# Kernel tuning notes

Hardware: AMD Instinct MI355X
Metric: run time of the kernel (lower is better)

The kernel has to match this reference:

```python
import jax, jax.numpy as jnp
import numpy as np

T, B, S, V = 50, 64, 400, 50000
D = 512; E = 512; H = 512; A = 512; POOL = 2


def setup_inputs() -> dict:
    key = jax.random.key(0)
    ks = jax.random.split(key, 20)
    def rn(k, shape, s=0.05):
        return jax.random.normal(k, shape, jnp.float32) * s
    return {
        "input_y": jax.random.randint(ks[0], (T, B), 0, V),
        "hidden": rn(ks[1], (1, B, H), 1.0),
        "context": rn(ks[2], (S, B, E), 1.0),
        "src_pad_mask": jnp.zeros((B, S), jnp.float32),
        "init_att": rn(ks[3], (B, E), 1.0),
        "coverage": jnp.zeros((B, S), jnp.float32),
        "global_ctx": rn(ks[4], (B, E), 1.0),
        "emb_W": rn(ks[5], (V, D)).at[0].set(0.0),  # padding_idx=0
        "W_ih": rn(ks[6], (3 * H, D + E)),
        "W_hh": rn(ks[7], (3 * H, H)),
        "b_ih": jnp.zeros((3 * H,), jnp.float32),
        "b_hh": jnp.zeros((3 * H,), jnp.float32),
        "W_pre": rn(ks[8], (E, A)),
        "b_pre": jnp.zeros((A,), jnp.float32),
        "W_q": rn(ks[9], (H + E, A)),
        "W_v": rn(ks[10], (A,)),
        "W_cov": rn(ks[11], (A,)),
        "W_pgen": rn(ks[12], (E + H + D,)),
        "b_pgen": jnp.zeros((), jnp.float32),
        "W_ro": rn(ks[13], (D + H + E + E, H)),
        "b_ro": jnp.zeros((H,), jnp.float32),
    }


def _gru_cell(x, h, W_ih, W_hh, b_ih, b_hh):
    # PyTorch GRUCell gate order: r, z, n
    gi = x @ W_ih.T + b_ih
    gh = h @ W_hh.T + b_hh
    i_r, i_z, i_n = jnp.split(gi, 3, axis=-1)
    h_r, h_z, h_n = jnp.split(gh, 3, axis=-1)
    r = jax.nn.sigmoid(i_r + h_r)
    z = jax.nn.sigmoid(i_z + h_z)
    n = jnp.tanh(i_n + r * h_n)
    return (1.0 - z) * n + z * h


def reference(input_y, hidden, context, src_pad_mask, init_att, coverage, global_ctx,
              emb_W, W_ih, W_hh, b_ih, b_hh, W_pre, b_pre, W_q, W_v, W_cov,
              W_pgen, b_pgen, W_ro, b_ro):
    emb = emb_W[input_y]                      # [T,B,D]
    ctx = jnp.transpose(context, (1, 0, 2))   # [B,S,E]
    precompute = ctx @ W_pre + b_pre          # [B,S,A] (computed once, as in module)
    pad = src_pad_mask > 0.5
    NEG = jnp.float32(-1e18)

    def step(carry, emb_t):
        h, cur_ctx, cov = carry
        x = jnp.concatenate([emb_t, cur_ctx], 1)          # input feed
        h0 = _gru_cell(x, h[0], W_ih, W_hh, b_ih, b_hh)   # layers=1
        h = h.at[0].set(h0)
        output = h0
        # concat attention with coverage
        q = jnp.concatenate([output, global_ctx], 1) @ W_q          # [B,A]
        tmp = jnp.tanh(precompute + q[:, None, :] + cov[..., None] * W_cov)
        energy = tmp @ W_v                                           # [B,S]
        energy = jnp.where(pad, NEG, energy)
        attn = jax.nn.softmax(energy, axis=1)
        cur_ctx = jnp.einsum('bs,bse->be', attn, ctx)
        # pointer-gen
        p_gen = jax.nn.sigmoid(
            jnp.concatenate([cur_ctx, output, emb_t], 1) @ W_pgen + b_pgen)[:, None]
        # readout + maxout (dropout is identity in eval)
        readout = jnp.concatenate([emb_t, output, cur_ctx, global_ctx], 1) @ W_ro + b_ro
        mo = readout.reshape(B, H // POOL, POOL).max(axis=-1)        # [B,H/POOL]
        cov_loss = jnp.sum(jnp.minimum(attn, cov), 1)                # cov_loss_wt=1.0
        next_cov = cov + attn
        return (h, cur_ctx, next_cov), (mo, p_gen, attn, cov_loss)

    (hidden_f, cur_ctx_f, cov_f), (g_out, g_pg, g_attn, cov_losses) = jax.lax.scan(
        step, (hidden, init_att, coverage), emb)
    return (g_out, hidden_f, g_attn[-1], cur_ctx_f, g_pg, g_attn, cov_losses, cov_f)
```

## Files before the change

### kernel.cpp

```cpp
#include <hip/hip_runtime.h>
#include <hip/hip_bf16.h>


#define T_STEPS 50
#define BB 64
#define SS 400

#define O_GOUT 0
#define O_HID 819200
#define O_ATTN_LAST 851968
#define O_CTXF 877568
#define O_PG 910336
#define O_GATTN 913536
#define O_COVL 2193536
#define O_COVF 2196736

typedef __attribute__((ext_vector_type(4))) float f4;
typedef __attribute__((ext_vector_type(8))) short s8v;
typedef __attribute__((ext_vector_type(4))) unsigned u4;

static __device__ __forceinline__ float bf2f(unsigned short u){
  unsigned v = ((unsigned)u) << 16; return __builtin_bit_cast(float, v);
}
static __device__ __forceinline__ unsigned short f2bf(float f){
  unsigned u = __builtin_bit_cast(unsigned, f);
  unsigned r = (u + 0x7FFFu + ((u >> 16) & 1u)) >> 16;
  return (unsigned short)r;
}
static __device__ __forceinline__ float sigmoidf_(float x){ return 1.f/(1.f+__expf(-x)); }
static __device__ __forceinline__ float tanhf_(float x){ float e=__expf(2.f*x); return 1.f - 2.f/(e+1.f); }
static __device__ __forceinline__ float ald32f(const float* p){
  unsigned u = __hip_atomic_load((const unsigned*)p, __ATOMIC_RELAXED, __HIP_MEMORY_SCOPE_AGENT);
  return __builtin_bit_cast(float, u);
}
static __device__ __forceinline__ void ast32f(float* p, float v){
  __hip_atomic_store((unsigned*)p, __builtin_bit_cast(unsigned, v),
                     __ATOMIC_RELAXED, __HIP_MEMORY_SCOPE_AGENT);
}

__global__ void conv_ctx(const float* __restrict__ ctx, unsigned short* __restrict__ out){
  int o = blockIdx.x*256 + threadIdx.x;
  if(o >= SS*BB*512) return;
  int e = o & 511; int b = (o>>9)&63; int s = o>>15;
  out[((b*SS+s)<<9) + e] = f2bf(ctx[o]);
}
__global__ void conv_emb(const int* __restrict__ y, const float* __restrict__ embW,
                         unsigned short* __restrict__ embU){
  int o = blockIdx.x*256+threadIdx.x; if(o>=T_STEPS*BB*512) return;
  int d = o & 511; int i = o>>9;
  embU[o] = f2bf(embW[(long)y[i]*512 + d]);
}
__global__ void conv_rest(const float* __restrict__ W_ih, const float* __restrict__ W_hh,
                          const float* __restrict__ W_pre, const float* __restrict__ W_ro,
                          const float* __restrict__ W_q,
                          const float* __restrict__ hidden, const float* __restrict__ init_att,
                          const float* __restrict__ gctx, const float* __restrict__ coverage,
                          unsigned short* __restrict__ wihbf, unsigned short* __restrict__ wpreT,
                          unsigned short* __restrict__ wroT, unsigned short* __restrict__ Wgru,
                          unsigned short* __restrict__ WqP,
                          float* __restrict__ hrow0, unsigned short* __restrict__ h0bf_init,
                          unsigned short* __restrict__ ctx0bf, float* __restrict__ gctxT,
                          float* __restrict__ cov, unsigned* __restrict__ flags){
  int o = blockIdx.x*256+threadIdx.x;
  if(o < 786432){
    int j = o>>9; int d = o&511;
    wihbf[o] = f2bf(W_ih[(long)j*1024 + d]);
  } else if(o < 1048576){
    int p = o - 786432;
    int a = p>>9; int e = p&511;
    wpreT[p] = f2bf(W_pre[(long)e*512 + a]);
  } else if(o < 2097152){
    int p = o - 1048576;
    int n = p>>11; int k = p&2047;
    wroT[p] = f2bf(W_ro[(long)k*512 + n]);
  } else if(o < 3670016){
    int p = o - 2097152;
    int rg = p >> 13; int rem = p & 8191;
    int ki = rem >> 9; int ln = (rem >> 3) & 63; int e = p & 7;
    int blk = rg/24; int r2 = rg%24; int w = r2/6; int r3 = r2%6; int g = r3>>1; int op = r3&1;
    int rl = ln & 15; int kk = ((ln>>4)<<3) + e;
    int d = blk*64 + w*16 + rl; int j = g*512 + d; int k = ki*32 + kk;
    float v = op ? W_hh[(long)j*512 + k] : W_ih[(long)j*1024 + 512 + k];
    Wgru[p] = f2bf(v);
  } else if(o < 3932160){
    int p = o - 3670016;
    int e = p&7; int ln=(p>>3)&63; int kf=(p>>9)&1; int nrg=(p>>10)&31; int blk=p>>15;
    int n = nrg*16 + (ln&15);
    int k = blk*64 + kf*32 + ((ln>>4)<<3) + e;
    WqP[p] = f2bf(W_q[(long)k*512 + n]);
  } else if(o < 4056128){
    int p = o - 3932160;
    if(p < 32768){ float v = hidden[p]; hrow0[p] = v; h0bf_init[p] = f2bf(v); }
    else if(p < 65536){ int q=p-32768; ctx0bf[q] = f2bf(init_att[q]); }
    else if(p < 98304){ int q=p-65536; int b=q>>9,e=q&511; gctxT[e*64+b]=gctx[q]; }
    else if(p < 123904){ int q=p-98304; cov[q]=coverage[q]; }
    else { int q=p-123904; if(q<64) flags[q]=0u; }
  }
}

template<int OUT_BF16>
__global__ __launch_bounds__(256) void mfma_gemm(
    const unsigned short* __restrict__ Abf, int lda,
    const unsigned short* __restrict__ Bbf, int ldb,
    void* __restrict__ Cp, int ldc, const float* __restrict__ bias, int K)
{
  __shared__ __align__(16) unsigned short Ash[128*40];
  __shared__ __align__(16) unsigned short Bsh[128*40];
  int m0 = blockIdx.x*128, n0 = blockIdx.y*128;
  int tid = threadIdx.x;
  int wid = tid>>6, lane = tid&63;
  int wm = wid>>1, wn = wid&1;
  int lr = lane&15, lg = lane>>4;
  f4 acc[4][4];
  #pragma unroll
  for(int i=0;i<4;i++)
    #pragma unroll
    for(int j=0;j<4;j++) acc[i][j]=(f4)0.f;

  for(int kt=0; kt<K; kt+=32){
    #pragma unroll
    for(int c=0;c<2;c++){
      int flat = tid*16 + c*8;
      int row = flat>>5, col = flat&31;
      const unsigned short* ga = Abf + (long)(m0+row)*lda + kt + col;
      *(uint4*)(&Ash[row*40+col]) = *(const uint4*)ga;
      const unsigned short* gb = Bbf + (long)(n0+row)*ldb + kt + col;
      *(uint4*)(&Bsh[row*40+col]) = *(const uint4*)gb;
    }
    __syncthreads();
    s8v av[4], bv[4];
    #pragma unroll
    for(int mi=0;mi<4;mi++) av[mi] = *(const s8v*)(&Ash[(wm*64+mi*16+lr)*40 + lg*8]);
    #pragma unroll
    for(int ni=0;ni<4;ni++) bv[ni] = *(const s8v*)(&Bsh[(wn*64+ni*16+lr)*40 + lg*8]);
    #pragma unroll
    for(int mi=0;mi<4;mi++)
      #pragma unroll
      for(int ni=0;ni<4;ni++)
        acc[mi][ni] = __builtin_amdgcn_mfma_f32_16x16x32_bf16(av[mi], bv[ni], acc[mi][ni], 0,0,0);
    __syncthreads();
  }
  #pragma unroll
  for(int mi=0;mi<4;mi++)
    #pragma unroll
    for(int ni=0;ni<4;ni++){
      int gc = n0 + wn*64 + ni*16 + lr;
      #pragma unroll
      for(int r=0;r<4;r++){
        int gr = m0 + wm*64 + mi*16 + lg*4 + r;
        float v = acc[mi][ni][r];
        if(bias) v += bias[gc];
        if(OUT_BF16) ((unsigned short*)Cp)[(long)gr*ldc + gc] = f2bf(v);
        else         ((float*)Cp)[(long)gr*ldc + gc] = v;
      }
    }
}

__global__ __launch_bounds__(256) void mfma_gemm_ro(
    const unsigned short* __restrict__ embU, const unsigned short* __restrict__ h0bf,
    const unsigned short* __restrict__ ctxA, const unsigned short* __restrict__ wroT,
    float* __restrict__ RO, const float* __restrict__ bias)
{
  __shared__ __align__(16) unsigned short Ash[128*40];
  __shared__ __align__(16) unsigned short Bsh[128*40];
  int m0 = blockIdx.x*128, n0 = blockIdx.y*128;
  int tid = threadIdx.x;
  int wid = tid>>6, lane = tid&63;
  int wm = wid>>1, wn = wid&1;
  int lr = lane&15, lg = lane>>4;
  f4 acc[4][4];
  #pragma unroll
  for(int i=0;i<4;i++)
    #pragma unroll
    for(int j=0;j<4;j++) acc[i][j]=(f4)0.f;

  for(int kt=0; kt<1536; kt+=32){
    const unsigned short* src = (kt<512) ? embU : (kt<1024) ? h0bf : ctxA;
    int klocal = kt & 511;
    #pragma unroll
    for(int c=0;c<2;c++){
      int flat = tid*16 + c*8;
      int row = flat>>5, col = flat&31;
      *(uint4*)(&Ash[row*40+col]) = *(const uint4*)(src + (long)(m0+row)*512 + klocal + col);
      *(uint4*)(&Bsh[row*40+col]) = *(const uint4*)(wroT + (long)(n0+row)*2048 + kt + col);
    }
    __syncthreads();
    s8v av[4], bv[4];
    #pragma unroll
    for(int mi=0;mi<4;mi++) av[mi] = *(const s8v*)(&Ash[(wm*64+mi*16+lr)*40 + lg*8]);
    #pragma unroll
    for(int ni=0;ni<4;ni++) bv[ni] = *(const s8v*)(&Bsh[(wn*64+ni*16+lr)*40 + lg*8]);
    #pragma unroll
    for(int mi=0;mi<4;mi++)
      #pragma unroll
      for(int ni=0;ni<4;ni++)
        acc[mi][ni] = __builtin_amdgcn_mfma_f32_16x16x32_bf16(av[mi], bv[ni], acc[mi][ni], 0,0,0);
    __syncthreads();
  }
  #pragma unroll
  for(int mi=0;mi<4;mi++)
    #pragma unroll
    for(int ni=0;ni<4;ni++){
      int gc = n0 + wn*64 + ni*16 + lr;
      #pragma unroll
      for(int r=0;r<4;r++){
        int gr = m0 + wm*64 + mi*16 + lg*4 + r;
        RO[(long)gr*512 + gc] = acc[mi][ni][r] + bias[gc];
      }
    }
}

__global__ __launch_bounds__(256) void small2(
  const float* __restrict__ AT, const float* __restrict__ W_q, const float* __restrict__ W_ro,
  float* __restrict__ q_g, float* __restrict__ ro_g)
{
  int blk = blockIdx.x;
  int half = blk>>7; int nblk = blk&127;
  int tid = threadIdx.x;
  int b = tid&63; int nq = tid>>6;
  int n = __builtin_amdgcn_readfirstlane(nblk*4 + nq);
  const float* W = half ? W_ro : W_q;
  int koff = half ? 1536 : 512;
  float acc = 0.f;
  const float* wp = W + (long)koff*512 + n;
  #pragma unroll 8
  for(int k=0;k<512;k++){
    acc = fmaf(AT[k*64+b], wp[(long)k*512], acc);
  }
  (half ? ro_g : q_g)[b*512+n] = acc;
}

__global__ __launch_bounds__(512) void k_step(
  const unsigned short* __restrict__ ctx0bf, float* __restrict__ ctxP,
  float* __restrict__ S_part, float* __restrict__ P_exp,
  const unsigned short* __restrict__ hprevbf,
  const float* __restrict__ hrow_in, float* __restrict__ hrow_out,
  const unsigned short* __restrict__ Wp, const unsigned short* __restrict__ WqP,
  const float* __restrict__ gi_emb, const float* __restrict__ b_hh,
  unsigned short* __restrict__ h0bf_all, float* __restrict__ qpart,
  float* __restrict__ cov, unsigned short* __restrict__ ctxA,
  const unsigned short* __restrict__ pre, const unsigned short* __restrict__ ctxbf,
  const float* __restrict__ q_g, const float* __restrict__ Wv,
  const float* __restrict__ Wcov, const float* __restrict__ padm,
  float* __restrict__ covl_part, unsigned* __restrict__ flags,
  float* __restrict__ outp, int t)
{
  __shared__ __align__(16) char smem[75008];
  const int blk = blockIdx.x;
  const int tid = threadIdx.x;
  const int w = tid>>6, lane = tid&63;
  const int lr = lane&15, lg = lane>>4;

  if(blk < 8){
    unsigned short* Ash = (unsigned short*)smem;
    unsigned short* HS  = (unsigned short*)(smem+65536);
    float* invS = (float*)(smem+74752);
    const int swz = (lr&7)<<4;
    const int dg = w&3, bh = w>>2;
    const int rgbase = blk*24 + dg*6;

    if(t>0 && tid<64){
      const float* Sp = S_part + ((t-1)&1)*256 + tid*4;
      invS[tid] = 1.f/(Sp[0]+Sp[1]+Sp[2]+Sp[3]);
    }
    __syncthreads();

    f4 acc2[6][2];
    #pragma unroll
    for(int u=0;u<6;u++)
      #pragma unroll
      for(int mm=0;mm<2;mm++) acc2[u][mm]=(f4)0.f;

    for(int kp=0; kp<2; kp++){
      for(int c = tid; c < 4096; c += 512){
        int op = c>>11; int row = (c>>5)&63; int kc = c&31;
        int e0 = kp*256 + kc*8;
        u4 v;
        if(op){
          v = *(const u4*)(hprevbf + row*512 + e0);
        } else if(t>0){
          const float* cp = ctxP + (long)row*2048 + e0;
          float sc = invS[row];
          f4 a0 = *(const f4*)(cp);
          f4 a1 = *(const f4*)(cp+512);
          f4 a2 = *(const f4*)(cp+1024);
          f4 a3 = *(const f4*)(cp+1536);
          f4 b0 = *(const f4*)(cp+4);
          f4 b1 = *(const f4*)(cp+516);
          f4 b2 = *(const f4*)(cp+1028);
          f4 b3 = *(const f4*)(cp+1540);
          f4 s0 = (a0+a1+a2+a3)*sc;
          f4 s1 = (b0+b1+b2+b3)*sc;
          v.x = (unsigned)f2bf(s0.x) | ((unsigned)f2bf(s0.y)<<16);
          v.y = (unsigned)f2bf(s0.z) | ((unsigned)f2bf(s0.w)<<16);
          v.z = (unsigned)f2bf(s1.x) | ((unsigned)f2bf(s1.y)<<16);
          v.w = (unsigned)f2bf(s1.z) | ((unsigned)f2bf(s1.w)<<16);
          if(blk == (row>>3))
            *(u4*)(ctxA + ((long)((t-1)*64+row))*512 + e0) = v;
        } else {
          v = *(const u4*)(ctx0bf + row*512 + e0);
        }
        int dst = op*32768 + row*512 + ((kc*16) ^ ((row&7)<<4));
        *(u4*)((char*)Ash + dst) = v;
      }
      __syncthreads();
      {
        #pragma unroll 2
        for(int ktl=0; ktl<256; ktl+=32){
          s8v av[2][2];
          #pragma unroll
          for(int op=0;op<2;op++)
            #pragma unroll
            for(int mm=0;mm<2;mm++){
              int mi = bh*2+mm;
              av[op][mm] = *(const s8v*)((const char*)Ash + op*32768 + (mi*16+lr)*512 + ((ktl*2 + lg*16) ^ swz));
            }
          int ki = kp*8 + (ktl>>5);
          const unsigned short* wb = Wp + (long)rgbase*8192 + ki*512 + lane*8;
          #pragma unroll
          for(int u=0;u<6;u++){
            s8v bv = *(const s8v*)(wb + (long)u*8192);
            #pragma unroll
            for(int mm=0;mm<2;mm++)
              acc2[u][mm] = __builtin_amdgcn_mfma_f32_16x16x32_bf16(av[u&1][mm], bv, acc2[u][mm], 0,0,0);
          }
        }
      }
      __syncthreads();
    }

    {
      int d = blk*64 + dg*16 + lr;
      float bhr = b_hh[d], bhz = b_hh[512+d], bhn = b_hh[1024+d];
      #pragma unroll
      for(int mm=0;mm<2;mm++){
        int mi = bh*2+mm;
        #pragma unroll
        for(int r=0;r<4;r++){
          int b = mi*16 + lg*4 + r;
          const float* ge = gi_emb + (long)(t*64+b)*1536;
          float g0 = __builtin_nontemporal_load(ge + d);
          float g1 = __builtin_nontemporal_load(ge + 512 + d);
          float g2 = __builtin_nontemporal_load(ge + 1024 + d);
          float rr = sigmoidf_(g0 + bhr + acc2[0][mm][r] + acc2[1][mm][r]);
          float zz = sigmoidf_(g1 + bhz + acc2[2][mm][r] + acc2[3][mm][r]);
          float nn = tanhf_(  g2       + acc2[4][mm][r] + rr*(acc2[5][mm][r] + bhn));
          float hp = hrow_in[b*512 + d];
          float hv = (1.f-zz)*nn + zz*hp;
          hrow_out[b*512+d] = hv;
          unsigned short hb = f2bf(hv);
          h0bf_all[(long)(t*64+b)*512 + d] = hb;
          HS[b*72 + dg*16 + lr] = hb;
          if(t==T_STEPS-1) outp[O_HID + b*512 + d] = hv;
        }
      }
    }
    __syncthreads();
    {
      #pragma unroll
      for(int i=0;i<8;i++){
        f4 accq[2];
        accq[0]=(f4)0.f; accq[1]=(f4)0.f;
        #pragma unroll
        for(int kf=0;kf<2;kf++){
          s8v bv = *(const s8v*)(WqP + ((((long)blk*32 + (dg*8+i))*2 + kf)*64 + lane)*8);
          #pragma unroll
          for(int mm=0;mm<2;mm++){
            int mi = bh*2+mm;
            s8v av = *(const s8v*)(HS + (mi*16+lr)*72 + kf*32 + lg*8);
            accq[mm] = __builtin_amdgcn_mfma_f32_16x16x32_bf16(av, bv, accq[mm], 0,0,0);
          }
        }
        int n = dg*128 + i*16 + lr;
        #pragma unroll
        for(int mm=0;mm<2;mm++)
          #pragma unroll
          for(int r=0;r<4;r++)
            ast32f(qpart + (long)blk*32768 + (long)((bh*2+mm)*16+lg*4+r)*512 + n, accq[mm][r]);
      }
    }
    asm volatile("s_waitcnt vmcnt(0)" ::: "memory");
    __syncthreads();
    if(tid==0)
      __hip_atomic_fetch_add(flags+t, 1u, __ATOMIC_RELEASE, __HIP_MEMORY_SCOPE_AGENT);
    return;
  }

  {
    int eb = blk-8; int b = eb>>2, cq = eb&3, c0 = cq*100;
    float* q_sh  = (float*)smem;
    float* wv_sh = (float*)(smem+2048);
    float* wc_sh = (float*)(smem+4096);
    float* covL  = (float*)(smem+6144);
    float* padL  = (float*)(smem+6560);
    float* red   = (float*)(smem+7392);
    float* red2  = (float*)(smem+9440);
    float* pb    = (float*)(smem+9472);

    wv_sh[tid]=Wv[tid]; wc_sh[tid]=Wcov[tid];
    if(tid<100) padL[tid]=padm[b*400+c0+tid];
    float clp = 0.f;
    if(t>0){
      const float* Sp = S_part + ((t-1)&1)*256 + b*4;
      float inv = 1.f/(Sp[0]+Sp[1]+Sp[2]+Sp[3]);
      if(tid<100){
        float p = P_exp[b*400+c0+tid]*inv;
        float co = cov[b*400+c0+tid];
        clp = fminf(p,co);
        float nc = co+p;
        cov[b*400+c0+tid]=nc;
        covL[tid]=nc;
        outp[O_GATTN + (long)(t-1)*25600 + b*400 + c0 + tid] = p;
      }
    } else {
      if(tid<100) covL[tid]=cov[b*400+c0+tid];
    }
    const unsigned short* prow = pre   + (((long)(b*400+c0))<<9) + lane*8;
    const unsigned short* crow = ctxbf + (((long)(b*400+c0))<<9) + lane*8;
    u4 pr[13], cr[13];
    #pragma unroll
    for(int j=0;j<13;j++){
      int i = w + j*8;
      long ro = (long)((i<100)? i : 0) << 9;
      pr[j] = *(const u4*)(prow + ro);
      cr[j] = *(const u4*)(crow + ro);
    }
    red[tid]=clp; __syncthreads();
    for(int o=256;o;o>>=1){ if(tid<o) red[tid]+=red[tid+o]; __syncthreads(); }
    if(t>0 && tid==0) covl_part[(long)(t-1)*256 + b*4+cq] = red[0];
    if(tid==0){
      unsigned it=0;
      while(__hip_atomic_load(flags+t, __ATOMIC_RELAXED, __HIP_MEMORY_SCOPE_AGENT) < 8u){
        __builtin_amdgcn_s_sleep(8);
        if(++it > 200000000u) break;
      }
    }
    __syncthreads();
    asm volatile("" ::: "memory");
    {
      float acc = q_g[b*512+tid];
      #pragma unroll
      for(int p=0;p<8;p++) acc += ald32f(qpart + ((long)p<<15) + b*512 + tid);
      q_sh[tid] = acc;
    }
    __syncthreads();
    float wsum = 0.f;
    float acc8[8];
    #pragma unroll
    for(int j=0;j<8;j++) acc8[j]=0.f;
    #pragma unroll
    for(int j=0;j<13;j++){
      int i = w + j*8;
      if(i<100){
        u4 cur = pr[j];
        const unsigned* uu = (const unsigned*)&cur;
        float cv = covL[i];
        float part = 0.f;
        #pragma unroll
        for(int q4=0;q4<4;q4++){
          int a = lane*8 + q4*2;
          part += wv_sh[a]  * tanhf_(bf2f((unsigned short)(uu[q4]&0xffffu)) + q_sh[a]   + cv*wc_sh[a]);
          part += wv_sh[a+1]* tanhf_(bf2f((unsigned short)(uu[q4]>>16))    + q_sh[a+1] + cv*wc_sh[a+1]);
        }
        #pragma unroll
        for(int off=32;off;off>>=1) part += __shfl_xor(part, off, 64);
        float e = (padL[i]>0.5f) ? -1e18f : part;
        float p = __expf(e);
        if(lane==0) P_exp[b*400+c0+i] = p;
        wsum += p;
        u4 cc = cr[j];
        const unsigned* cu = (const unsigned*)&cc;
        acc8[0] = fmaf(p, bf2f((unsigned short)(cu[0]&0xffffu)), acc8[0]);
        acc8[1] = fmaf(p, bf2f((unsigned short)(cu[0]>>16)),     acc8[1]);
        acc8[2] = fmaf(p, bf2f((unsigned short)(cu[1]&0xffffu)), acc8[2]);
        acc8[3] = fmaf(p, bf2f((unsigned short)(cu[1]>>16)),     acc8[3]);
        acc8[4] = fmaf(p, bf2f((unsigned short)(cu[2]&0xffffu)), acc8[4]);
        acc8[5] = fmaf(p, bf2f((unsigned short)(cu[2]>>16)),     acc8[5]);
        acc8[6] = fmaf(p, bf2f((unsigned short)(cu[3]&0xffffu)), acc8[6]);
        acc8[7] = fmaf(p, bf2f((unsigned short)(cu[3]>>16)),     acc8[7]);
      }
    }
    if(lane==0) red2[w]=wsum;
    __syncthreads();
    if(tid==0)
      S_part[(t&1)*256 + b*4+cq] = red2[0]+red2[1]+red2[2]+red2[3]+red2[4]+red2[5]+red2[6]+red2[7];
    #pragma unroll
    for(int j=0;j<8;j++) pb[w*512 + lane*8+j] = acc8[j];
    __syncthreads();
    {
      float v = pb[tid]+pb[512+tid]+pb[1024+tid]+pb[1536+tid]
               +pb[2048+tid]+pb[2560+tid]+pb[3072+tid]+pb[3584+tid];
      ctxP[((long)b*4+cq)*512 + tid] = v;
    }
  }
}

__global__ __launch_bounds__(256) void k_fin(
  const float* __restrict__ ctxP, const float* __restrict__ S_part,
  const float* __restrict__ P_exp, const float* __restrict__ cov,
  const float* __restrict__ covl_part,
  unsigned short* __restrict__ ctxA, float* __restrict__ outp)
{
  __shared__ float red[256];
  int b = blockIdx.x; int tid = threadIdx.x;
  const int tb = T_STEPS-1;
  const float* Sp = S_part + 256 + b*4;
  float S = Sp[0]+Sp[1]+Sp[2]+Sp[3];
  float inv = 1.f/S;
  float clp;
  {
    float p = P_exp[b*400+tid]*inv;
    float co = cov[b*400+tid];
    clp = fminf(p, co);
    float nc = co+p;
    outp[O_GATTN + (long)tb*25600 + b*400 + tid] = p;
    outp[O_ATTN_LAST + b*400 + tid] = p;
    outp[O_COVF + b*400 + tid] = nc;
  }
  if(tid<144){
    int i = 256+tid;
    float p = P_exp[b*400+i]*inv;
    float co = cov[b*400+i];
    clp += fminf(p, co);
    float nc = co+p;
    outp[O_GATTN + (long)tb*25600 + b*400 + i] = p;
    outp[O_ATTN_LAST + b*400 + i] = p;
    outp[O_COVF + b*400 + i] = nc;
  }
  red[tid]=clp; __syncthreads();
  for(int o=128;o;o>>=1){ if(tid<o) red[tid]+=red[tid+o]; __syncthreads(); }
  if(tid==0) outp[O_COVL + tb*64 + b] = red[0];
  if(tid<49){
    const float* cp = covl_part + (long)tid*256 + b*4;
    outp[O_COVL + tid*64 + b] = cp[0]+cp[1]+cp[2]+cp[3];
  }
  for(int c=tid;c<512;c+=256){
    float v = (ctxP[(long)b*2048+c]+ctxP[(long)b*2048+512+c]
              +ctxP[(long)b*2048+1024+c]+ctxP[(long)b*2048+1536+c])*inv;
    outp[O_CTXF + b*512 + c] = v;
    ctxA[(long)(tb*64+b)*512 + c] = f2bf(v);
  }
}

__global__ __launch_bounds__(256) void k_post(
  const unsigned short* __restrict__ embU, const unsigned short* __restrict__ h0bf,
  const unsigned short* __restrict__ ctxA, const float* __restrict__ Wpg,
  const float* __restrict__ bpg, const float* __restrict__ RO,
  const float* __restrict__ ro_g, float* __restrict__ outp)
{
  int blk = blockIdx.x;
  if(blk < 800){
    int wid = threadIdx.x>>6, lane=threadIdx.x&63;
    int m = blk*4 + wid;
    float acc=0.f;
    #pragma unroll
    for(int i=0;i<8;i++){
      int k = i*64+lane;
      acc = fmaf(bf2f(ctxA[(long)m*512+k]), Wpg[k], acc);
      acc = fmaf(bf2f(h0bf[(long)m*512+k]), Wpg[512+k], acc);
      acc = fmaf(bf2f(embU[(long)m*512+k]), Wpg[1024+k], acc);
    }
    #pragma unroll
    for(int off=32; off; off>>=1) acc += __shfl_xor(acc, off, 64);
    if(lane==0) outp[O_PG + m] = sigmoidf_(acc + bpg[0]);
  } else {
    int o = (blk-800)*256 + threadIdx.x;
    int h = o & 255; int m = o>>8; int b = m & 63;
    float v0 = RO[(long)m*512 + 2*h]   + ro_g[b*512 + 2*h];
    float v1 = RO[(long)m*512 + 2*h+1] + ro_g[b*512 + 2*h+1];
    outp[O_GOUT + o] = fmaxf(v0,v1);
  }
}

extern "C" void kernel_launch(void* const* d_in, const int* in_sizes, int n_in,
                              void* d_out, int out_size, void* d_ws, size_t ws_size,
                              hipStream_t stream)
{
  (void)in_sizes; (void)n_in; (void)out_size; (void)ws_size;
  const int*   y       = (const int*)d_in[0];
  const float* hidden  = (const float*)d_in[1];
  const float* context = (const float*)d_in[2];
  const float* padm    = (const float*)d_in[3];
  const float* init_att= (const float*)d_in[4];
  const float* coverage= (const float*)d_in[5];
  const float* gctx    = (const float*)d_in[6];
  const float* embW    = (const float*)d_in[7];
  const float* W_ih    = (const float*)d_in[8];
  const float* W_hh    = (const float*)d_in[9];
  const float* b_ih    = (const float*)d_in[10];
  const float* b_hh    = (const float*)d_in[11];
  const float* W_pre   = (const float*)d_in[12];
  const float* b_pre   = (const float*)d_in[13];
  const float* W_q     = (const float*)d_in[14];
  const float* W_v     = (const float*)d_in[15];
  const float* W_cov   = (const float*)d_in[16];
  const float* W_pg    = (const float*)d_in[17];
  const float* b_pg    = (const float*)d_in[18];
  const float* W_ro    = (const float*)d_in[19];
  const float* b_ro    = (const float*)d_in[20];
  float* out = (float*)d_out;

  char* wsb = (char*)d_ws;
  size_t off = 0;
  auto alloc = [&](size_t bytes)->char*{ char* p = wsb+off; off += (bytes+255)&~255UL; return p; };
  unsigned short* pre    = (unsigned short*)alloc(25600UL*512*2);
  unsigned short* ctxbf  = (unsigned short*)alloc(13107200UL*2);
  unsigned short* embU   = (unsigned short*)alloc(3200UL*512*2);
  unsigned short* wihbf  = (unsigned short*)alloc(1536UL*512*2);
  unsigned short* wpreT  = (unsigned short*)alloc(512UL*512*2);
  unsigned short* wroT   = (unsigned short*)alloc(512UL*2048*2);
  unsigned short* Wgru   = (unsigned short*)alloc(192UL*8192*2);
  unsigned short* WqP    = (unsigned short*)alloc(262144UL*2);
  float* gi_emb = (float*)alloc(3200UL*1536*4);
  float* RO     = (float*)alloc(3200UL*512*4);
  float* q_g    = (float*)alloc(64UL*512*4);
  float* ro_g   = (float*)alloc(64UL*512*4);
  float* hrow0  = (float*)alloc(64UL*512*4);
  float* hrow1  = (float*)alloc(64UL*512*4);
  float* gctxT  = (float*)alloc(512UL*64*4);
  unsigned short* h0bf = (unsigned short*)alloc(3200UL*512*2);
  unsigned short* h0bf_init = (unsigned short*)alloc(64UL*512*2);
  unsigned short* ctx0bf    = (unsigned short*)alloc(64UL*512*2);
  unsigned short* ctxA = (unsigned short*)alloc(3200UL*512*2);
  float* ctxP   = (float*)alloc(64UL*4*512*4);
  float* P_exp  = (float*)alloc(64UL*400*4);
  float* S_part = (float*)alloc(2UL*256*4);
  float* qpart  = (float*)alloc(8UL*64*512*4);
  float* cov    = (float*)alloc(64UL*400*4);
  float* covl_part = (float*)alloc(50UL*256*4);
  unsigned* flags = (unsigned*)alloc(64UL*4);

  conv_ctx <<<dim3(51200),dim3(256),0,stream>>>(context, ctxbf);
  conv_emb <<<dim3(6400), dim3(256),0,stream>>>(y, embW, embU);
  conv_rest<<<dim3(15845),dim3(256),0,stream>>>(W_ih, W_hh, W_pre, W_ro, W_q,
                                                hidden, init_att, gctx, coverage,
                                                wihbf, wpreT, wroT, Wgru, WqP,
                                                hrow0, h0bf_init, ctx0bf, gctxT, cov, flags);

  mfma_gemm<1><<<dim3(200,4),dim3(256),0,stream>>>(ctxbf,512, wpreT,512,  pre,   512, b_pre, 512);
  mfma_gemm<0><<<dim3(25,12),dim3(256),0,stream>>>(embU, 512, wihbf,512,  gi_emb,1536, b_ih, 512);
  small2<<<dim3(256),dim3(256),0,stream>>>(gctxT, W_q, W_ro, q_g, ro_g);

  for(int t=0; t<T_STEPS; t++){
    float* hin  = (t&1) ? hrow1 : hrow0;
    float* hout = (t&1) ? hrow0 : hrow1;
    const unsigned short* hprevbf = t ? (h0bf + (long)(t-1)*32768) : h0bf_init;
    k_step<<<dim3(264),dim3(512),0,stream>>>(ctx0bf, ctxP, S_part, P_exp, hprevbf,
                                             hin, hout, Wgru, WqP, gi_emb, b_hh,
                                             h0bf, qpart, cov, ctxA, pre, ctxbf,
                                             q_g, W_v, W_cov, padm, covl_part,
                                             flags, out, t);
  }

  k_fin<<<dim3(64),dim3(256),0,stream>>>(ctxP, S_part, P_exp, cov, covl_part, ctxA, out);
  mfma_gemm_ro<<<dim3(25,4),dim3(256),0,stream>>>(embU, h0bf, ctxA, wroT, RO, b_ro);
  k_post<<<dim3(4000),dim3(256),0,stream>>>(embU, h0bf, ctxA, W_pg, b_pg, RO, ro_g, out);
}
```

Baseline: 2.779 ms.

## Split context reduction into 64 dedicated blocks with flag handoff to GRU blocks

Before, each of the 8 GRU blocks reduced the four attention-context partials for all 64 rows and converted them to bf16, so the same work was repeated 8 times. Now 64 extra blocks each reduce one batch row, write a bf16 ctxR buffer plus the ctxA history, and bump a per-step flag. The GRU blocks spin on that flag and then load the finished bf16 rows. This removes the redundant reduction but adds a cross-block spin-wait and extra launched blocks, and the spin iteration limits were lowered.

```diff
diff --git a/kernel.cpp b/kernel.cpp
--- a/kernel.cpp
+++ b/kernel.cpp
@@ -18,6 +18,7 @@
 typedef __attribute__((ext_vector_type(4))) float f4;
 typedef __attribute__((ext_vector_type(8))) short s8v;
 typedef __attribute__((ext_vector_type(4))) unsigned u4;
+typedef unsigned long long u64;
 
 static __device__ __forceinline__ float bf2f(unsigned short u){
   unsigned v = ((unsigned)u) << 16; return __builtin_bit_cast(float, v);
@@ -36,6 +37,12 @@
 static __device__ __forceinline__ void ast32f(float* p, float v){
   __hip_atomic_store((unsigned*)p, __builtin_bit_cast(unsigned, v),
                      __ATOMIC_RELAXED, __HIP_MEMORY_SCOPE_AGENT);
+}
+static __device__ __forceinline__ u64 ald64(const void* p){
+  return __hip_atomic_load((const u64*)p, __ATOMIC_RELAXED, __HIP_MEMORY_SCOPE_AGENT);
+}
+static __device__ __forceinline__ void ast64(void* p, u64 v){
+  __hip_atomic_store((u64*)p, v, __ATOMIC_RELAXED, __HIP_MEMORY_SCOPE_AGENT);
 }
 
 __global__ void conv_ctx(const float* __restrict__ ctx, unsigned short* __restrict__ out){
@@ -88,13 +95,13 @@
     int n = nrg*16 + (ln&15);
     int k = blk*64 + kf*32 + ((ln>>4)<<3) + e;
     WqP[p] = f2bf(W_q[(long)k*512 + n]);
-  } else if(o < 4056128){
+  } else if(o < 4056192){
     int p = o - 3932160;
     if(p < 32768){ float v = hidden[p]; hrow0[p] = v; h0bf_init[p] = f2bf(v); }
     else if(p < 65536){ int q=p-32768; ctx0bf[q] = f2bf(init_att[q]); }
     else if(p < 98304){ int q=p-65536; int b=q>>9,e=q&511; gctxT[e*64+b]=gctx[q]; }
     else if(p < 123904){ int q=p-98304; cov[q]=coverage[q]; }
-    else { int q=p-123904; if(q<64) flags[q]=0u; }
+    else { int q=p-123904; if(q<128) flags[q]=0u; }
   }
 }
 
@@ -239,6 +246,7 @@
   const float* __restrict__ gi_emb, const float* __restrict__ b_hh,
   unsigned short* __restrict__ h0bf_all, float* __restrict__ qpart,
   float* __restrict__ cov, unsigned short* __restrict__ ctxA,
+  unsigned short* __restrict__ ctxR,
   const unsigned short* __restrict__ pre, const unsigned short* __restrict__ ctxbf,
   const float* __restrict__ q_g, const float* __restrict__ Wv,
   const float* __restrict__ Wcov, const float* __restrict__ padm,
@@ -251,19 +259,49 @@
   const int w = tid>>6, lane = tid&63;
   const int lr = lane&15, lg = lane>>4;
 
-  if(blk < 8){
+  if(blk < 64){
+    if(t==0) return;
+    int b = blk; int tb = t-1;
+    if(tid < 128){
+      const float* Sp = S_part + (tb&1)*256 + b*4;
+      float inv = 1.f/(Sp[0]+Sp[1]+Sp[2]+Sp[3]);
+      int e0 = tid*4;
+      const float* cp = ctxP + (long)b*2048 + e0;
+      f4 p0 = *(const f4*)cp;
+      f4 p1 = *(const f4*)(cp+512);
+      f4 p2 = *(const f4*)(cp+1024);
+      f4 p3 = *(const f4*)(cp+1536);
+      f4 s = (p0+p1+p2+p3)*inv;
+      u64 v = (u64)f2bf(s.x) | ((u64)f2bf(s.y)<<16) | ((u64)f2bf(s.z)<<32) | ((u64)f2bf(s.w)<<48);
+      ast64(ctxR + b*512 + e0, v);
+      *(u64*)(ctxA + (long)(tb*64+b)*512 + e0) = v;
+    }
+    asm volatile("s_waitcnt vmcnt(0)" ::: "memory");
+    __syncthreads();
+    if(tid==0)
+      __hip_atomic_fetch_add(flags+64+t, 1u, __ATOMIC_RELEASE, __HIP_MEMORY_SCOPE_AGENT);
+    return;
+  }
+
+  if(blk < 72){
+    int gblk = blk - 64;
     unsigned short* Ash = (unsigned short*)smem;
     unsigned short* HS  = (unsigned short*)(smem+65536);
-    float* invS = (float*)(smem+74752);
     const int swz = (lr&7)<<4;
     const int dg = w&3, bh = w>>2;
-    const int rgbase = blk*24 + dg*6;
-
-    if(t>0 && tid<64){
-      const float* Sp = S_part + ((t-1)&1)*256 + tid*4;
-      invS[tid] = 1.f/(Sp[0]+Sp[1]+Sp[2]+Sp[3]);
-    }
-    __syncthreads();
+    const int rgbase = gblk*24 + dg*6;
+
+    if(t>0){
+      if(tid==0){
+        unsigned it=0;
+        while(__hip_atomic_load(flags+64+t, __ATOMIC_RELAXED, __HIP_MEMORY_SCOPE_AGENT) < 64u){
+          __builtin_amdgcn_s_sleep(2);
+          if(++it > 20000000u) break;
+        }
+      }
+      __syncthreads();
+      asm volatile("" ::: "memory");
+    }
 
     f4 acc2[6][2];
     #pragma unroll
@@ -279,24 +317,10 @@
         if(op){
           v = *(const u4*)(hprevbf + row*512 + e0);
         } else if(t>0){
-          const float* cp = ctxP + (long)row*2048 + e0;
-          float sc = invS[row];
-          f4 a0 = *(const f4*)(cp);
-          f4 a1 = *(const f4*)(cp+512);
-          f4 a2 = *(const f4*)(cp+1024);
-          f4 a3 = *(const f4*)(cp+1536);
-          f4 b0 = *(const f4*)(cp+4);
-          f4 b1 = *(const f4*)(cp+516);
-          f4 b2 = *(const f4*)(cp+1028);
-          f4 b3 = *(const f4*)(cp+1540);
-          f4 s0 = (a0+a1+a2+a3)*sc;
-          f4 s1 = (b0+b1+b2+b3)*sc;
-          v.x = (unsigned)f2bf(s0.x) | ((unsigned)f2bf(s0.y)<<16);
-          v.y = (unsigned)f2bf(s0.z) | ((unsigned)f2bf(s0.w)<<16);
-          v.z = (unsigned)f2bf(s1.x) | ((unsigned)f2bf(s1.y)<<16);
-          v.w = (unsigned)f2bf(s1.z) | ((unsigned)f2bf(s1.w)<<16);
-          if(blk == (row>>3))
-            *(u4*)(ctxA + ((long)((t-1)*64+row))*512 + e0) = v;
+          u64 lo = ald64(ctxR + row*512 + e0);
+          u64 hi = ald64(ctxR + row*512 + e0 + 4);
+          v.x = (unsigned)lo; v.y = (unsigned)(lo>>32);
+          v.z = (unsigned)hi; v.w = (unsigned)(hi>>32);
         } else {
           v = *(const u4*)(ctx0bf + row*512 + e0);
         }
@@ -330,7 +354,7 @@
     }
 
     {
-      int d = blk*64 + dg*16 + lr;
+      int d = gblk*64 + dg*16 + lr;
       float bhr = b_hh[d], bhz = b_hh[512+d], bhn = b_hh[1024+d];
       #pragma unroll
       for(int mm=0;mm<2;mm++){
@@ -363,7 +387,7 @@
         accq[0]=(f4)0.f; accq[1]=(f4)0.f;
         #pragma unroll
         for(int kf=0;kf<2;kf++){
-          s8v bv = *(const s8v*)(WqP + ((((long)blk*32 + (dg*8+i))*2 + kf)*64 + lane)*8);
+          s8v bv = *(const s8v*)(WqP + ((((long)gblk*32 + (dg*8+i))*2 + kf)*64 + lane)*8);
           #pragma unroll
           for(int mm=0;mm<2;mm++){
             int mi = bh*2+mm;
@@ -376,7 +400,7 @@
         for(int mm=0;mm<2;mm++)
           #pragma unroll
           for(int r=0;r<4;r++)
-            ast32f(qpart + (long)blk*32768 + (long)((bh*2+mm)*16+lg*4+r)*512 + n, accq[mm][r]);
+            ast32f(qpart + (long)gblk*32768 + (long)((bh*2+mm)*16+lg*4+r)*512 + n, accq[mm][r]);
       }
     }
     asm volatile("s_waitcnt vmcnt(0)" ::: "memory");
@@ -387,7 +411,7 @@
   }
 
   {
-    int eb = blk-8; int b = eb>>2, cq = eb&3, c0 = cq*100;
+    int eb = blk-72; int b = eb>>2, cq = eb&3, c0 = cq*100;
     float* q_sh  = (float*)smem;
     float* wv_sh = (float*)(smem+2048);
     float* wc_sh = (float*)(smem+4096);
@@ -432,7 +456,7 @@
       unsigned it=0;
       while(__hip_atomic_load(flags+t, __ATOMIC_RELAXED, __HIP_MEMORY_SCOPE_AGENT) < 8u){
         __builtin_amdgcn_s_sleep(8);
-        if(++it > 200000000u) break;
+        if(++it > 20000000u) break;
       }
     }
     __syncthreads();
@@ -622,13 +646,14 @@
   unsigned short* h0bf_init = (unsigned short*)alloc(64UL*512*2);
   unsigned short* ctx0bf    = (unsigned short*)alloc(64UL*512*2);
   unsigned short* ctxA = (unsigned short*)alloc(3200UL*512*2);
+  unsigned short* ctxR = (unsigned short*)alloc(64UL*512*2);
   float* ctxP   = (float*)alloc(64UL*4*512*4);
   float* P_exp  = (float*)alloc(64UL*400*4);
   float* S_part = (float*)alloc(2UL*256*4);
   float* qpart  = (float*)alloc(8UL*64*512*4);
   float* cov    = (float*)alloc(64UL*400*4);
   float* covl_part = (float*)alloc(50UL*256*4);
-  unsigned* flags = (unsigned*)alloc(64UL*4);
+  unsigned* flags = (unsigned*)alloc(128UL*4);
 
   conv_ctx <<<dim3(51200),dim3(256),0,stream>>>(context, ctxbf);
   conv_emb <<<dim3(6400), dim3(256),0,stream>>>(y, embW, embU);
@@ -645,9 +670,9 @@
     float* hin  = (t&1) ? hrow1 : hrow0;
     float* hout = (t&1) ? hrow0 : hrow1;
     const unsigned short* hprevbf = t ? (h0bf + (long)(t-1)*32768) : h0bf_init;
-    k_step<<<dim3(264),dim3(512),0,stream>>>(ctx0bf, ctxP, S_part, P_exp, hprevbf,
+    k_step<<<dim3(328),dim3(512),0,stream>>>(ctx0bf, ctxP, S_part, P_exp, hprevbf,
                                              hin, hout, Wgru, WqP, gi_emb, b_hh,
-                                             h0bf, qpart, cov, ctxA, pre, ctxbf,
+                                             h0bf, qpart, cov, ctxA, ctxR, pre, ctxbf,
                                              q_g, W_v, W_cov, padm, covl_part,
                                              flags, out, t);
   }
```

Result: no change. 2.759 ms (-0.7%).
